# Performance work log

Measured on AMD Instinct MI355X. Metric: run time of the kernel, lower is better.

Reference implementation:

```python
import math
import jax, jax.numpy as jnp
import numpy as np
from jax import lax

LEAKY_SLOPE = 0.2
ACT_GAIN = math.sqrt(2.0)

def bilinear_filter():
    h = jnp.array([1.0, 3.0, 3.0, 1.0], dtype=jnp.float32)
    h = h[:, None] * h[None, :]
    return h / jnp.sum(h)

def setup_inputs() -> dict:
    key = jax.random.key(0)
    ks = jax.random.split(key, 6)
    B, Cin, Cout, W_DIM, R = 16, 512, 512, 512, 64
    return {
        "x": jax.random.normal(ks[0], (B, Cin, R // 2, R // 2), dtype=jnp.float32),
        "w": jax.random.normal(ks[1], (B, W_DIM), dtype=jnp.float32),
        "noise_raw": jax.random.normal(ks[2], (B, 1, R, R), dtype=jnp.float32),
        "affine_weight": jax.random.normal(ks[3], (Cin, W_DIM), dtype=jnp.float32),
        "affine_bias": jnp.ones((Cin,), dtype=jnp.float32),
        "weight": jax.random.normal(ks[4], (Cout, Cin, 3, 3), dtype=jnp.float32),
        "bias": 0.1 * jax.random.normal(ks[5], (Cout,), dtype=jnp.float32),
        "noise_strength": jnp.float32(1.0),
    }

def reference(x, w, noise_raw, affine_weight, affine_bias, weight, bias, noise_strength):
    B, Cin = x.shape[0], x.shape[1]
    Cout = weight.shape[0]
    w_dim = affine_weight.shape[1]
    # EqualizedLinear affine: weight_gain = 1/sqrt(in), bias_gain = 1, no activation
    styles = w @ (affine_weight * (1.0 / math.sqrt(w_dim))).T + affine_bias  # [B, Cin]
    # demodulation coefficients from modulated weights
    wmod = weight[None] * styles[:, None, :, None, None]                      # [B,Cout,Cin,3,3]
    dcoefs = lax.rsqrt(jnp.sum(jnp.square(wmod), axis=(2, 3, 4)) + 1e-8)     # [B, Cout]
    # modulate input instead of weights
    xs = x * styles[:, :, None, None]
    # up=True path: conv_transpose2d(x, weight.transpose(0,1), stride=2, padding=0)
    # == dilated conv with spatially flipped kernel, pad k-1=2
    w_flip = weight[:, :, ::-1, ::-1]
    y = lax.conv_general_dilated(
        xs, w_flip, window_strides=(1, 1), padding=[(2, 2), (2, 2)],
        lhs_dilation=(2, 2), dimension_numbers=("NCHW", "OIHW", "NCHW"))    # [B,Cout,2H+1,2H+1]
    # filter2d with 4x4 bilinear kernel, gain=4, padding=1 (depthwise)
    f = bilinear_filter() * 4.0
    kd = jnp.tile(f[None, None], (Cout, 1, 1, 1))                            # [Cout,1,4,4]
    y = lax.conv_general_dilated(
        y, kd, window_strides=(1, 1), padding=[(1, 1), (1, 1)],
        dimension_numbers=("NCHW", "OIHW", "NCHW"), feature_group_count=Cout)  # [B,Cout,2H,2H]
    # addcmul: noise + y * dcoefs
    noise = noise_raw * noise_strength
    y = noise + y * dcoefs[:, :, None, None]
    # bias, act gain sqrt(2), leaky relu 0.2
    y = (y + bias[None, :, None, None]) * ACT_GAIN
    return jnp.where(y >= 0, y, LEAKY_SLOPE * y)
```

## Files before the change

kernel.cpp:

```cpp
#include <hip/hip_runtime.h>
#include <hip/hip_bf16.h>
#include <stdint.h>

typedef float f32x4 __attribute__((ext_vector_type(4)));
typedef __bf16 bf16x8 __attribute__((ext_vector_type(8)));

#define GLDS16(gp, lp) __builtin_amdgcn_global_load_lds( \
    (const __attribute__((address_space(1))) void*)(gp), \
    (__attribute__((address_space(3))) void*)(lp), 16, 0, 0)

static __device__ __forceinline__ unsigned short f2bf(float f) {
    unsigned int u = __float_as_uint(f);
    u = (u + 0x7fffu + ((u >> 16) & 1u)) >> 16;
    return (unsigned short)u;
}
static __device__ __forceinline__ float bf2f(unsigned short v) {
    return __uint_as_float(((unsigned int)v) << 16);
}

#define O_STYLES 0
#define O_DCOEF  32768
#define O_XS     65536
#define O_WP     19005440
#define O_Y1     23724032
#define O_WSQ    23724032
#define WS_NEED  96075776
#define SP 1104

__global__ __launch_bounds__(256) void k_styles(const float* __restrict__ w,
                                                const float* __restrict__ aw,
                                                const float* __restrict__ ab,
                                                float* __restrict__ styles) {
    int g = blockIdx.x * 256 + threadIdx.x;
    int b = g >> 9, ci = g & 511;
    const float4* wr = (const float4*)(w + b * 512);
    const float4* ar = (const float4*)(aw + ci * 512);
    float acc = 0.f;
    for (int k = 0; k < 128; ++k) {
        float4 wv = wr[k], av = ar[k];
        acc += wv.x * av.x + wv.y * av.y + wv.z * av.z + wv.w * av.w;
    }
    styles[g] = acc * 0.04419417382415922f + ab[ci];
}

__global__ __launch_bounds__(256) void k_wprep(const float* __restrict__ weight,
                                               float* __restrict__ wsq,
                                               unsigned short* __restrict__ wp) {
    int g = blockIdx.x * 256 + threadIdx.x;
    const float* wb = weight + (long)g * 9;
    float v[9]; float s = 0.f;
#pragma unroll
    for (int t = 0; t < 9; ++t) { v[t] = wb[t]; s += v[t] * v[t]; }
    wsq[g] = s;
    const int wri[9] = {2, 2, 0, 0, 2, 0, 1, 1, 1};
    const int wci[9] = {2, 0, 2, 0, 1, 1, 2, 0, 1};
#pragma unroll
    for (int t = 0; t < 9; ++t)
        wp[t * 262144 + g] = f2bf(v[wri[t] * 3 + wci[t]]);
}

__global__ __launch_bounds__(256) void k_dcoef(const float* __restrict__ styles,
                                               const float* __restrict__ wsq,
                                               float* __restrict__ dcoefs) {
    int g = blockIdx.x * 256 + threadIdx.x;
    int b = g >> 9, co = g & 511;
    const float4* sr = (const float4*)(styles + b * 512);
    const float4* qr = (const float4*)(wsq + co * 512);
    float acc = 1e-8f;
    for (int k = 0; k < 128; ++k) {
        float4 sv = sr[k], qv = qr[k];
        acc += sv.x * sv.x * qv.x + sv.y * sv.y * qv.y + sv.z * sv.z * qv.z + sv.w * sv.w * qv.w;
    }
    dcoefs[g] = rsqrtf(acc);
}

__global__ __launch_bounds__(256) void k_xprep(const float* __restrict__ x,
                                               const float* __restrict__ styles,
                                               unsigned short* __restrict__ xs) {
    __shared__ float T[128][33];
    int bid = blockIdx.x;
    int cc = bid & 3, i = (bid >> 2) & 31, b = bid >> 7;
    int t = threadIdx.x;
    int ci0 = cc * 128;
    int j_r = t & 31, cl_r = t >> 5;
    const float* xp = x + (((long)(b * 512 + ci0)) * 32 + i) * 32;
#pragma unroll
    for (int it = 0; it < 16; ++it) {
        int cl = cl_r + it * 8;
        T[cl][j_r] = xp[cl * 1024 + j_r];
    }
    __syncthreads();
    int ci_w = t & 127, jg = t >> 7;
    float sv = styles[b * 512 + ci0 + ci_w];
    unsigned short* op = xs + (((long)(b * 34 + (i + 1))) * 34 + 1) * 512 + ci0 + ci_w;
#pragma unroll
    for (int jj = 0; jj < 16; ++jj) {
        int j = jg * 16 + jj;
        op[(long)j * 512] = f2bf(T[ci_w][j] * sv);
    }
}

#define ST_A(kk) { GLDS16(xsB + sA0 + akt + (kk)*64, smp + nb + (kk)*16384 + t16); \
                   GLDS16(xsB + sA1 + akt + (kk)*64, smp + nb + (kk)*16384 + t16 + 8192); }
#define ST_B(kk) { GLDS16(wpB + sB0 + bkt + (kk)*64, smp + nb + 32768 + (kk)*16384 + t16); \
                   GLDS16(wpB + sB1 + bkt + (kk)*64, smp + nb + 32768 + (kk)*16384 + t16 + 8192); }
#define PHASE2(kk, STG, TAILBAR) { \
  _Pragma("unroll") for (int i = 0; i < 8; ++i) \
    av[i] = *(const bf16x8*)(smp + cb + (kk)*16384 + abase + (i*16)*64); \
  _Pragma("unroll") for (int j = 0; j < 4; ++j) \
    bv[j] = *(const bf16x8*)(smp + cb + (kk)*16384 + bbase + (j*16)*64); \
  STG; \
  __builtin_amdgcn_sched_barrier(0); \
  asm volatile("s_waitcnt vmcnt(4)" ::: "memory"); \
  __builtin_amdgcn_s_barrier(); \
  asm volatile("s_waitcnt lgkmcnt(0)" ::: "memory"); \
  __builtin_amdgcn_sched_barrier(0); \
  __builtin_amdgcn_s_setprio(1); \
  _Pragma("unroll") for (int i = 0; i < 8; ++i) \
    _Pragma("unroll") for (int j = 0; j < 4; ++j) \
      acc[i][j] = __builtin_amdgcn_mfma_f32_16x16x32_bf16(av[i], bv[j], acc[i][j], 0, 0, 0); \
  __builtin_amdgcn_s_setprio(0); \
  if (TAILBAR) __builtin_amdgcn_s_barrier(); }

__global__ __launch_bounds__(512, 2) void k_conv(const unsigned short* __restrict__ xs,
                                                 const unsigned short* __restrict__ wp,
                                                 unsigned short* __restrict__ y1) {
    extern __shared__ __align__(16) char smem[];
    const unsigned char* xsB = (const unsigned char*)xs;
    const unsigned char* wpB = (const unsigned char*)wp;
    char* smp = smem;

    int bid = blockIdx.x;
    int par, q;
    if (bid < 138)      { par = 0; q = bid; }
    else if (bid < 276) { par = 1; q = bid - 138; }
    else if (bid < 414) { par = 2; q = bid - 276; }
    else                { par = 3; q = bid - 414; }
    int Mtile = q >> 1, Ntile = q & 1;
    int a_par = par >> 1, c_par = par & 1;
    int ntaps = a_par ? (c_par ? 1 : 2) : (c_par ? 2 : 4);
    int tapofs = (par == 0) ? 0 : ((par == 1) ? 4 : ((par == 2) ? 6 : 8));
    int NKT = ntaps << 3;

    int tid = threadIdx.x;
    int lane = tid & 63, wave = tid >> 6;
    int wm = wave >> 2, wn = wave & 3;
    int lrow = lane & 15;
    int rchunk = (((lane >> 4) ^ ((lrow >> 1) & 3)) << 4);
    int abase = (wm * 128 + lrow) * 64 + rchunk;
    int bbase = 32768 + (wn * 64 + lrow) * 64 + rchunk;

    int srow = tid >> 2;
    int schunk = (((tid & 3) ^ ((tid >> 3) & 3)) << 4);
    int sA0, sA1;
    {
        unsigned gm = (unsigned)(Mtile * 256 + srow);
        if (gm > 17471u) gm = 17471u;
        unsigned b_ = gm / 1092u; unsigned pix = gm - b_ * 1092u;
        unsigned r = pix / 33u; unsigned s = pix - r * 33u;
        sA0 = (int)(((b_ * 34u + r) * 34u + s) << 10) + schunk;
        gm = (unsigned)(Mtile * 256 + srow + 128);
        if (gm > 17471u) gm = 17471u;
        b_ = gm / 1092u; pix = gm - b_ * 1092u;
        r = pix / 33u; s = pix - r * 33u;
        sA1 = (int)(((b_ * 34u + r) * 34u + s) << 10) + schunk;
    }
    int sB0 = ((Ntile * 256 + srow) << 10) + schunk;
    int sB1 = sB0 + (128 << 10);
    int t16 = tid << 4;

    f32x4 acc[8][4];
#pragma unroll
    for (int i = 0; i < 8; ++i)
#pragma unroll
        for (int j = 0; j < 4; ++j)
            acc[i][j] = (f32x4){0.f, 0.f, 0.f, 0.f};
    bf16x8 av[8], bv[4];

    auto mkA = [&](int kt) -> int {
        int tl = kt >> 3; if (tl >= ntaps) tl = ntaps - 1;
        int cib = kt & 7;
        int dio = a_par ? 1 : (c_par ? tl : (tl >> 1));
        int djo = c_par ? 1 : (a_par ? tl : (tl & 1));
        return dio * 34816 + djo * 1024 + cib * 128;
    };
    auto mkB = [&](int kt) -> long {
        int tl = kt >> 3; if (tl >= ntaps) tl = ntaps - 1;
        return (long)(tapofs + tl) * 524288 + (long)((kt & 7) * 128);
    };

    {
        int akt = mkA(0); long bkt = mkB(0); int nb = 0;
        ST_A(0); ST_B(0); ST_A(1); ST_B(1);
    }
    __builtin_amdgcn_sched_barrier(0);
    asm volatile("s_waitcnt vmcnt(4)" ::: "memory");
    __builtin_amdgcn_s_barrier();

    int cur = 0;
    for (int kt = 0; kt < NKT; ++kt) {
        int akt = mkA(kt + 1);
        long bkt = mkB(kt + 1);
        int nb = (cur ^ 1) << 16;
        int cb = cur << 16;
        PHASE2(0, { ST_A(0); ST_B(0); }, 0)
        PHASE2(1, { ST_A(1); ST_B(1); }, 1)
        cur ^= 1;
    }

#pragma unroll
    for (int mf = 0; mf < 8; ++mf) {
        int gm0 = Mtile * 256 + wm * 128 + mf * 16 + ((lane >> 4) << 2);
        if (gm0 < 17472) {
            unsigned ug = (unsigned)gm0;
            unsigned bb = ug / 1092u;
            int pix0 = (int)(ug - bb * 1092u);
            long rowb = ((long)((bb * 4u + par) * 512) + 0) * SP;
#pragma unroll
            for (int nf = 0; nf < 4; ++nf) {
                int co = Ntile * 256 + wn * 64 + nf * 16 + lrow;
                ushort4 pk;
                pk.x = f2bf(acc[mf][nf][0]);
                pk.y = f2bf(acc[mf][nf][1]);
                pk.z = f2bf(acc[mf][nf][2]);
                pk.w = f2bf(acc[mf][nf][3]);
                *(ushort4*)(y1 + rowb + (long)co * SP + pix0) = pk;
            }
        }
    }
}

__global__ __launch_bounds__(256) void k_blur(const unsigned short* __restrict__ y1,
                                              const float* __restrict__ dcoefs,
                                              const float* __restrict__ bias,
                                              const float* __restrict__ noise,
                                              const float* __restrict__ nstr,
                                              float* __restrict__ out) {
    __shared__ float yl[67 * 69];
    int bid = blockIdx.x;
    int cg = bid & 63, b = bid >> 6;
    int t = threadIdx.x;
    int n = t & 63, mq = t >> 6;
    float ns = nstr[0];

    for (int i = t; i < 67 * 69; i += 256) yl[i] = 0.f;
    __syncthreads();

    const int Rv[4] = {33, 33, 32, 32};
    const int Sv[4] = {33, 32, 33, 32};
    const float* npb = noise + b * 4096;

    for (int cc = 0; cc < 8; ++cc) {
        int co = cg * 8 + cc;
#pragma unroll
        for (int pl = 0; pl < 4; ++pl) {
            int ap = pl >> 1, cq = pl & 1;
            const unsigned short* src = y1 + ((long)((b * 4 + pl) * 512 + co)) * SP;
            int rv = Rv[pl], sv = Sv[pl];
            for (int it = t; it < 273; it += 256) {
                int p0 = it * 4;
                ushort4 v = *(const ushort4*)(src + p0);
                unsigned short vv[4] = {v.x, v.y, v.z, v.w};
#pragma unroll
                for (int k = 0; k < 4; ++k) {
                    int p = p0 + k;
                    if (p < 1089) {
                        int r = p / 33;
                        int s = p - r * 33;
                        if (r < rv && s < sv)
                            yl[(2 * r + ap + 1) * 69 + (2 * s + cq + 1)] = bf2f(vv[k]);
                    }
                }
            }
        }
        __syncthreads();

        float dc = dcoefs[b * 512 + co];
        float bi = bias[co];
        int m0 = mq * 16;
        const float* r0p = &yl[(m0 - 1 + 1) * 69 + n];
        const float* r1p = r0p + 69;
        const float* r2p = r1p + 69;
        float t0 = (r0p[0] + r0p[3]) + 3.f * (r0p[1] + r0p[2]);
        float t1 = (r1p[0] + r1p[3]) + 3.f * (r1p[1] + r1p[2]);
        float t2 = (r2p[0] + r2p[3]) + 3.f * (r2p[1] + r2p[2]);
        float* ob = out + ((long)(b * 512 + co)) * 4096;
#pragma unroll
        for (int k = 0; k < 16; ++k) {
            int m = m0 + k;
            const float* rp = &yl[(m + 3) * 69 + n];
            float t3 = (rp[0] + rp[3]) + 3.f * (rp[1] + rp[2]);
            float a = (t0 + t3) + 3.f * (t1 + t2);
            float val = npb[m * 64 + n] * ns + a * (0.0625f * dc);
            val = (val + bi) * 1.41421356237309515f;
            ob[m * 64 + n] = (val >= 0.f) ? val : 0.2f * val;
            t0 = t1; t1 = t2; t2 = t3;
        }
        __syncthreads();
    }
}

extern "C" void kernel_launch(void* const* d_in, const int* in_sizes, int n_in,
                              void* d_out, int out_size, void* d_ws, size_t ws_size,
                              hipStream_t stream) {
    (void)in_sizes; (void)n_in; (void)out_size;
    if (ws_size < (size_t)WS_NEED) return;
    const float* x      = (const float*)d_in[0];
    const float* w      = (const float*)d_in[1];
    const float* noise  = (const float*)d_in[2];
    const float* aw     = (const float*)d_in[3];
    const float* ab     = (const float*)d_in[4];
    const float* weight = (const float*)d_in[5];
    const float* bias   = (const float*)d_in[6];
    const float* nstr   = (const float*)d_in[7];
    float* out = (float*)d_out;
    char* ws = (char*)d_ws;
    float* styles          = (float*)(ws + O_STYLES);
    float* dcoefs          = (float*)(ws + O_DCOEF);
    unsigned short* xs     = (unsigned short*)(ws + O_XS);
    unsigned short* wp     = (unsigned short*)(ws + O_WP);
    unsigned short* y1     = (unsigned short*)(ws + O_Y1);
    float* wsq             = (float*)(ws + O_WSQ);

    hipFuncSetAttribute((const void*)k_conv,
                        hipFuncAttributeMaxDynamicSharedMemorySize, 131072);

    hipMemsetAsync(xs, 0, 18939904, stream);
    k_styles<<<32,   256, 0, stream>>>(w, aw, ab, styles);
    k_wprep <<<1024, 256, 0, stream>>>(weight, wsq, wp);
    k_dcoef <<<32,   256, 0, stream>>>(styles, wsq, dcoefs);
    k_xprep <<<2048, 256, 0, stream>>>(x, styles, xs);
    k_conv  <<<552,  512, 131072, stream>>>(xs, wp, y1);
    k_blur  <<<1024, 256, 0, stream>>>(y1, dcoefs, bias, noise, nstr, out);
}
```

Baseline: 212.6 us.

## Deepen conv LDS pipeline to 4 stages and restructure blur into per-parity polyphase planes

```diff
diff --git a/kernel.cpp b/kernel.cpp
--- a/kernel.cpp
+++ b/kernel.cpp
@@ -100,27 +100,11 @@
     }
 }
 
-#define ST_A(kk) { GLDS16(xsB + sA0 + akt + (kk)*64, smp + nb + (kk)*16384 + t16); \
-                   GLDS16(xsB + sA1 + akt + (kk)*64, smp + nb + (kk)*16384 + t16 + 8192); }
-#define ST_B(kk) { GLDS16(wpB + sB0 + bkt + (kk)*64, smp + nb + 32768 + (kk)*16384 + t16); \
-                   GLDS16(wpB + sB1 + bkt + (kk)*64, smp + nb + 32768 + (kk)*16384 + t16 + 8192); }
-#define PHASE2(kk, STG, TAILBAR) { \
-  _Pragma("unroll") for (int i = 0; i < 8; ++i) \
-    av[i] = *(const bf16x8*)(smp + cb + (kk)*16384 + abase + (i*16)*64); \
-  _Pragma("unroll") for (int j = 0; j < 4; ++j) \
-    bv[j] = *(const bf16x8*)(smp + cb + (kk)*16384 + bbase + (j*16)*64); \
-  STG; \
-  __builtin_amdgcn_sched_barrier(0); \
-  asm volatile("s_waitcnt vmcnt(4)" ::: "memory"); \
-  __builtin_amdgcn_s_barrier(); \
-  asm volatile("s_waitcnt lgkmcnt(0)" ::: "memory"); \
-  __builtin_amdgcn_sched_barrier(0); \
-  __builtin_amdgcn_s_setprio(1); \
-  _Pragma("unroll") for (int i = 0; i < 8; ++i) \
-    _Pragma("unroll") for (int j = 0; j < 4; ++j) \
-      acc[i][j] = __builtin_amdgcn_mfma_f32_16x16x32_bf16(av[i], bv[j], acc[i][j], 0, 0, 0); \
-  __builtin_amdgcn_s_setprio(0); \
-  if (TAILBAR) __builtin_amdgcn_s_barrier(); }
+#define ST4(hh, slot) { int _a = mkA(hh); long _b = mkB(hh); \
+  GLDS16(xsB + sA0 + _a, smp + (slot)*16384 + t16); \
+  GLDS16(xsB + sA1 + _a, smp + (slot)*16384 + t16 + 8192); \
+  GLDS16(wpB + sB0 + _b, smp + 65536 + (slot)*16384 + t16); \
+  GLDS16(wpB + sB1 + _b, smp + 65536 + (slot)*16384 + t16 + 8192); }
 
 __global__ __launch_bounds__(512, 2) void k_conv(const unsigned short* __restrict__ xs,
                                                  const unsigned short* __restrict__ wp,
@@ -140,7 +124,7 @@
     int a_par = par >> 1, c_par = par & 1;
     int ntaps = a_par ? (c_par ? 1 : 2) : (c_par ? 2 : 4);
     int tapofs = (par == 0) ? 0 : ((par == 1) ? 4 : ((par == 2) ? 6 : 8));
-    int NKT = ntaps << 3;
+    int HMAX = ntaps << 4;
 
     int tid = threadIdx.x;
     int lane = tid & 63, wave = tid >> 6;
@@ -148,7 +132,7 @@
     int lrow = lane & 15;
     int rchunk = (((lane >> 4) ^ ((lrow >> 1) & 3)) << 4);
     int abase = (wm * 128 + lrow) * 64 + rchunk;
-    int bbase = 32768 + (wn * 64 + lrow) * 64 + rchunk;
+    int bbase = (wn * 64 + lrow) * 64 + rchunk;
 
     int srow = tid >> 2;
     int schunk = (((tid & 3) ^ ((tid >> 3) & 3)) << 4);
@@ -177,35 +161,51 @@
             acc[i][j] = (f32x4){0.f, 0.f, 0.f, 0.f};
     bf16x8 av[8], bv[4];
 
-    auto mkA = [&](int kt) -> int {
+    auto mkA = [&](int h) -> int {
+        int kt = h >> 1, kk = h & 1;
         int tl = kt >> 3; if (tl >= ntaps) tl = ntaps - 1;
         int cib = kt & 7;
         int dio = a_par ? 1 : (c_par ? tl : (tl >> 1));
         int djo = c_par ? 1 : (a_par ? tl : (tl & 1));
-        return dio * 34816 + djo * 1024 + cib * 128;
+        return dio * 34816 + djo * 1024 + cib * 128 + kk * 64;
     };
-    auto mkB = [&](int kt) -> long {
+    auto mkB = [&](int h) -> long {
+        int kt = h >> 1, kk = h & 1;
         int tl = kt >> 3; if (tl >= ntaps) tl = ntaps - 1;
-        return (long)(tapofs + tl) * 524288 + (long)((kt & 7) * 128);
+        return (long)(tapofs + tl) * 524288 + (long)((kt & 7) * 128 + kk * 64);
     };
 
-    {
-        int akt = mkA(0); long bkt = mkB(0); int nb = 0;
-        ST_A(0); ST_B(0); ST_A(1); ST_B(1);
-    }
+    ST4(0, 0); ST4(1, 1); ST4(2, 2);
     __builtin_amdgcn_sched_barrier(0);
-    asm volatile("s_waitcnt vmcnt(4)" ::: "memory");
+    asm volatile("s_waitcnt vmcnt(8)" ::: "memory");
     __builtin_amdgcn_s_barrier();
 
-    int cur = 0;
-    for (int kt = 0; kt < NKT; ++kt) {
-        int akt = mkA(kt + 1);
-        long bkt = mkB(kt + 1);
-        int nb = (cur ^ 1) << 16;
-        int cb = cur << 16;
-        PHASE2(0, { ST_A(0); ST_B(0); }, 0)
-        PHASE2(1, { ST_A(1); ST_B(1); }, 1)
-        cur ^= 1;
+    for (int h = 0; h < HMAX; ++h) {
+        int s = h & 3;
+        const char* Ab = smp + s * 16384;
+        const char* Bb = smp + 65536 + s * 16384;
+#pragma unroll
+        for (int i = 0; i < 8; ++i)
+            av[i] = *(const bf16x8*)(Ab + abase + i * 1024);
+#pragma unroll
+        for (int j = 0; j < 4; ++j)
+            bv[j] = *(const bf16x8*)(Bb + bbase + j * 1024);
+        int hs = h + 3; if (hs > HMAX - 1) hs = HMAX - 1;
+        int ss = (h + 3) & 3;
+        ST4(hs, ss);
+        __builtin_amdgcn_sched_barrier(0);
+        asm volatile("s_waitcnt vmcnt(8)" ::: "memory");
+        __builtin_amdgcn_s_barrier();
+        asm volatile("s_waitcnt lgkmcnt(0)" ::: "memory");
+        __builtin_amdgcn_sched_barrier(0);
+        __builtin_amdgcn_s_setprio(1);
+#pragma unroll
+        for (int i = 0; i < 8; ++i)
+#pragma unroll
+            for (int j = 0; j < 4; ++j)
+                acc[i][j] = __builtin_amdgcn_mfma_f32_16x16x32_bf16(av[i], bv[j], acc[i][j], 0, 0, 0);
+        __builtin_amdgcn_s_setprio(0);
+        __builtin_amdgcn_s_barrier();
     }
 
 #pragma unroll
@@ -215,16 +215,23 @@
             unsigned ug = (unsigned)gm0;
             unsigned bb = ug / 1092u;
             int pix0 = (int)(ug - bb * 1092u);
-            long rowb = ((long)((bb * 4u + par) * 512) + 0) * SP;
+            unsigned rr = (unsigned)pix0 % 33u;
+            long rowb = ((long)((bb * 4u + par) * 512)) * SP;
 #pragma unroll
             for (int nf = 0; nf < 4; ++nf) {
                 int co = Ntile * 256 + wn * 64 + nf * 16 + lrow;
-                ushort4 pk;
-                pk.x = f2bf(acc[mf][nf][0]);
-                pk.y = f2bf(acc[mf][nf][1]);
-                pk.z = f2bf(acc[mf][nf][2]);
-                pk.w = f2bf(acc[mf][nf][3]);
-                *(ushort4*)(y1 + rowb + (long)co * SP + pix0) = pk;
+                if (pix0 <= 1084) {
+                    ushort4 pk;
+                    pk.x = f2bf(acc[mf][nf][0]);
+                    pk.y = f2bf(acc[mf][nf][1]);
+                    pk.z = f2bf(acc[mf][nf][2]);
+                    pk.w = f2bf(acc[mf][nf][3]);
+                    if (c_par && rr >= 29)
+                        ((unsigned short*)&pk)[32 - rr] = 0;
+                    *(ushort4*)(y1 + rowb + (long)co * SP + pix0) = pk;
+                } else if (pix0 == 1088) {
+                    y1[rowb + (long)co * SP + 1088] = c_par ? (unsigned short)0 : f2bf(acc[mf][nf][0]);
+                }
             }
         }
     }
@@ -236,27 +243,32 @@
                                               const float* __restrict__ noise,
                                               const float* __restrict__ nstr,
                                               float* __restrict__ out) {
-    __shared__ float yl[67 * 69];
+    __shared__ float yl[4 * 35 * 36];
     int bid = blockIdx.x;
-    int cg = bid & 63, b = bid >> 6;
+    int cg = bid & 127, b = bid >> 7;
     int t = threadIdx.x;
     int n = t & 63, mq = t >> 6;
     float ns = nstr[0];
 
-    for (int i = t; i < 67 * 69; i += 256) yl[i] = 0.f;
+    for (int i = t; i < 5040; i += 256) yl[i] = 0.f;
     __syncthreads();
 
-    const int Rv[4] = {33, 33, 32, 32};
-    const int Sv[4] = {33, 32, 33, 32};
+    const int rvv[4] = {33, 33, 32, 32};
     const float* npb = noise + b * 4096;
 
-    for (int cc = 0; cc < 8; ++cc) {
-        int co = cg * 8 + cc;
+    int o = n & 1;
+    int se = n >> 1;
+    int sp_ = se - 1 + o;
+    float a0 = o ? 1.f : 3.f;
+    float a1 = o ? 3.f : 1.f;
+
+    for (int cc = 0; cc < 4; ++cc) {
+        int co = cg * 4 + cc;
 #pragma unroll
         for (int pl = 0; pl < 4; ++pl) {
-            int ap = pl >> 1, cq = pl & 1;
             const unsigned short* src = y1 + ((long)((b * 4 + pl) * 512 + co)) * SP;
-            int rv = Rv[pl], sv = Sv[pl];
+            float* dst = yl + pl * 1260;
+            int pv = rvv[pl] * 33;
             for (int it = t; it < 273; it += 256) {
                 int p0 = it * 4;
                 ushort4 v = *(const ushort4*)(src + p0);
@@ -264,11 +276,10 @@
 #pragma unroll
                 for (int k = 0; k < 4; ++k) {
                     int p = p0 + k;
-                    if (p < 1089) {
-                        int r = p / 33;
-                        int s = p - r * 33;
-                        if (r < rv && s < sv)
-                            yl[(2 * r + ap + 1) * 69 + (2 * s + cq + 1)] = bf2f(vv[k]);
+                    if (p < pv && p < 1089) {
+                        unsigned r = (unsigned)p / 33u;
+                        unsigned s = (unsigned)p - r * 33u;
+                        dst[(r + 1) * 36 + (s + 1)] = bf2f(vv[k]);
                     }
                 }
             }
@@ -277,24 +288,34 @@
 
         float dc = dcoefs[b * 512 + co];
         float bi = bias[co];
+        float* ob = out + ((long)(b * 512 + co)) * 4096;
+
+        auto H = [&](int ap, int r) -> float {
+            const float* pe = yl + (ap * 2) * 1260 + (r + 1) * 36;
+            const float* po = pe + 1260;
+            return a0 * pe[se + 1] + a1 * pe[se + 2] + a1 * po[sp_ + 1] + a0 * po[sp_ + 2];
+        };
+
         int m0 = mq * 16;
-        const float* r0p = &yl[(m0 - 1 + 1) * 69 + n];
-        const float* r1p = r0p + 69;
-        const float* r2p = r1p + 69;
-        float t0 = (r0p[0] + r0p[3]) + 3.f * (r0p[1] + r0p[2]);
-        float t1 = (r1p[0] + r1p[3]) + 3.f * (r1p[1] + r1p[2]);
-        float t2 = (r2p[0] + r2p[3]) + 3.f * (r2p[1] + r2p[2]);
-        float* ob = out + ((long)(b * 512 + co)) * 4096;
-#pragma unroll
-        for (int k = 0; k < 16; ++k) {
+        int re = m0 >> 1;
+        float he0 = H(0, re), he1 = H(0, re + 1);
+        float ho0 = H(1, re - 1), ho1 = H(1, re);
+#pragma unroll
+        for (int k = 0; k < 16; k += 2) {
             int m = m0 + k;
-            const float* rp = &yl[(m + 3) * 69 + n];
-            float t3 = (rp[0] + rp[3]) + 3.f * (rp[1] + rp[2]);
-            float a = (t0 + t3) + 3.f * (t1 + t2);
-            float val = npb[m * 64 + n] * ns + a * (0.0625f * dc);
+            float ve = 3.f * he0 + he1 + ho0 + 3.f * ho1;
+            float val = npb[m * 64 + n] * ns + ve * (0.0625f * dc);
             val = (val + bi) * 1.41421356237309515f;
             ob[m * 64 + n] = (val >= 0.f) ? val : 0.2f * val;
-            t0 = t1; t1 = t2; t2 = t3;
+            float hn_o = H(1, re + 1);
+            float vo = he0 + 3.f * he1 + 3.f * ho1 + hn_o;
+            val = npb[(m + 1) * 64 + n] * ns + vo * (0.0625f * dc);
+            val = (val + bi) * 1.41421356237309515f;
+            ob[(m + 1) * 64 + n] = (val >= 0.f) ? val : 0.2f * val;
+            ho0 = ho1; ho1 = hn_o;
+            float hn_e = H(0, re + 2);
+            he0 = he1; he1 = hn_e;
+            re += 1;
         }
         __syncthreads();
     }
@@ -331,5 +352,5 @@
     k_dcoef <<<32,   256, 0, stream>>>(styles, wsq, dcoefs);
     k_xprep <<<2048, 256, 0, stream>>>(x, styles, xs);
     k_conv  <<<552,  512, 131072, stream>>>(xs, wp, y1);
-    k_blur  <<<1024, 256, 0, stream>>>(y1, dcoefs, bias, noise, nstr, out);
-}
+    k_blur  <<<2048, 256, 0, stream>>>(y1, dcoefs, bias, noise, nstr, out);
+}
```

Result: slower. 222.3 us (+4.5%).
